# Performance work log

Hardware: AMD Instinct MI355X
Metric: run time of the kernel (lower is better)

## Reference

```python
import jax, jax.numpy as jnp
import numpy as np

B, S, D, H = 4, 2048, 1024, 16
HD = D // H

def setup_inputs() -> dict:
    key = jax.random.key(0)
    ks = jax.random.split(key, 11)
    s = 1.0 / np.sqrt(D)
    def lin(k):
        kw, kb = jax.random.split(k)
        return (jax.random.uniform(kw, (D, D), jnp.float32, -s, s),
                jax.random.uniform(kb, (D,), jnp.float32, -s, s))
    Wq, bq = lin(ks[0]); Wk, bk = lin(ks[1]); Wv, bv = lin(ks[2]); Wo, bo = lin(ks[3])
    return {
        "query": jax.random.normal(ks[4], (B, S, D), jnp.float32),
        "key": jax.random.normal(ks[5], (B, S, D), jnp.float32),
        "value": jax.random.normal(ks[6], (B, S, D), jnp.float32),
        "Wq": Wq, "bq": bq, "Wk": Wk, "bk": bk,
        "Wv": Wv, "bv": bv, "Wo": Wo, "bo": bo,
    }

def reference(query, key, value, Wq, bq, Wk, bk, Wv, bv, Wo, bo):
    def split_heads(x):  # [B,S,D] -> [B,H,S,HD]
        return x.reshape(B, S, H, HD).transpose(0, 2, 1, 3)
    q = split_heads(query @ Wq + bq)
    k = split_heads(key @ Wk + bk)
    v = split_heads(value @ Wv + bv)
    scores = jnp.einsum('bhqd,bhkd->bhqk', q, k) / np.sqrt(HD)
    probs = jax.nn.softmax(scores, axis=-1)
    ctx = jnp.einsum('bhqk,bhkd->bhqd', probs, v)
    ctx = ctx.transpose(0, 2, 1, 3).reshape(B, S, D)
    return ctx @ Wo + bo
```

## Files before the change

### kernel.cpp

```cpp
#include <hip/hip_runtime.h>
#include <hip/hip_bf16.h>

#define B_ 4
#define S_ 2048
#define D_ 1024
#define H_ 16
#define HD_ 64
#define M_ (B_*S_)

typedef __bf16 bf16;
typedef bf16 bf16x8 __attribute__((ext_vector_type(8)));
typedef bf16 bf16x4 __attribute__((ext_vector_type(4)));
typedef bf16 bf16x2 __attribute__((ext_vector_type(2)));
typedef float f32x4 __attribute__((ext_vector_type(4)));
typedef unsigned u32x4 __attribute__((ext_vector_type(4)));

__device__ __forceinline__ void gload_lds16(const void* g, void* l) {
  __builtin_amdgcn_global_load_lds((const __attribute__((address_space(1))) void*)g,
                                   (__attribute__((address_space(3))) void*)l, 16, 0, 0);
}

__device__ __forceinline__ unsigned pk2(float a, float b) {
  bf16x2 v;
  v[0] = (bf16)a; v[1] = (bf16)b;
  return __builtin_bit_cast(unsigned, v);
}

#define CVT_BLKS (M_ * D_ / 2048)

__global__ __launch_bounds__(256)
void prep_kernel(const float* __restrict__ q, const float* __restrict__ k,
                 const float* __restrict__ v,
                 bf16* __restrict__ qo, bf16* __restrict__ ko, bf16* __restrict__ vo,
                 const float* __restrict__ Wq, const float* __restrict__ Wk,
                 const float* __restrict__ Wv, const float* __restrict__ Wo,
                 bf16* __restrict__ Wqt, bf16* __restrict__ Wkt,
                 bf16* __restrict__ Wvt, bf16* __restrict__ Wot) {
  __shared__ float tile[64][65];
  const int bid = blockIdx.x;
  if (bid < 3 * CVT_BLKS) {
    const int slice = bid / CVT_BLKS, bx = bid % CVT_BLKS;
    const float* src; bf16* dst;
    if (slice == 0)      { src = q; dst = qo; }
    else if (slice == 1) { src = k; dst = ko; }
    else                 { src = v; dst = vo; }
    size_t i = ((size_t)bx * 256 + threadIdx.x) * 8;
    f32x4 a = *(const f32x4*)(src + i);
    f32x4 b = *(const f32x4*)(src + i + 4);
    bf16x8 o;
    o[0] = (bf16)a[0]; o[1] = (bf16)a[1]; o[2] = (bf16)a[2]; o[3] = (bf16)a[3];
    o[4] = (bf16)b[0]; o[5] = (bf16)b[1]; o[6] = (bf16)b[2]; o[7] = (bf16)b[3];
    *(bf16x8*)(dst + i) = o;
  } else {
    const int wb = bid - 3 * CVT_BLKS;
    const int z = wb >> 8, t = wb & 255;
    const float* W; bf16* Wt;
    switch (z) {
      case 0: W = Wq; Wt = Wqt; break;
      case 1: W = Wk; Wt = Wkt; break;
      case 2: W = Wv; Wt = Wvt; break;
      default: W = Wo; Wt = Wot; break;
    }
    const int n0 = (t & 15) * 64, k0 = (t >> 4) * 64;
    const int tx = threadIdx.x & 63, ty = threadIdx.x >> 6;
#pragma unroll
    for (int i = 0; i < 16; i++) {
      int kk = ty + i * 4;
      tile[kk][tx] = W[(size_t)(k0 + kk) * D_ + n0 + tx];
    }
    __syncthreads();
#pragma unroll
    for (int i = 0; i < 16; i++) {
      int n = ty + i * 4;
      Wt[(size_t)(n0 + n) * D_ + k0 + tx] = (bf16)tile[tx][n];
    }
  }
}

#define QSCALE 0.18033688011112042f

__global__ __launch_bounds__(256)
void proj_gemm_kernel(const bf16* __restrict__ Aqb, const bf16* __restrict__ Akb,
                      const bf16* __restrict__ Avb,
                      const bf16* __restrict__ Wqt, const bf16* __restrict__ Wkt,
                      const bf16* __restrict__ Wvt,
                      const float* __restrict__ bq, const float* __restrict__ bk,
                      const float* __restrict__ bv,
                      bf16* __restrict__ qb, bf16* __restrict__ kb, bf16* __restrict__ vbT) {
  __shared__ bf16 As[2][128 * 64];
  __shared__ bf16 Bs[2][128 * 64];
  const bf16* A; const bf16* Bt; const float* bias;
  if (blockIdx.z == 0)      { A = Aqb; Bt = Wqt; bias = bq; }
  else if (blockIdx.z == 1) { A = Akb; Bt = Wkt; bias = bk; }
  else                      { A = Avb; Bt = Wvt; bias = bv; }

  const int orig = blockIdx.y * gridDim.x + blockIdx.x;
  const int swz  = (orig & 7) * 64 + (orig >> 3);
  const int n0 = (swz & 7) * 128, m0 = (swz >> 3) * 128;

  const int tid = threadIdx.x;
  const int lane = tid & 63, w = tid >> 6;
  const int wr = w >> 1, wc = w & 1;
  const int l15 = lane & 15, quad = lane >> 4;
  const int srow = lane >> 3, schunk = lane & 7;

  f32x4 acc[4][4] = {};

  auto stage = [&](int buf, int kt) {
    const int k0 = kt * 64;
#pragma unroll
    for (int t = 0; t < 4; t++) {
      int r0 = w * 32 + t * 8;
      int row = r0 + srow;
      int cg = schunk ^ (row & 7);
      gload_lds16(A + (size_t)(m0 + row) * D_ + k0 + cg * 8, &As[buf][r0 * 64]);
      gload_lds16(Bt + (size_t)(n0 + row) * D_ + k0 + cg * 8, &Bs[buf][r0 * 64]);
    }
  };

  auto compute = [&](int cur) {
#pragma unroll
    for (int ks = 0; ks < 2; ks++) {
      bf16x8 a[4], b[4];
#pragma unroll
      for (int fm = 0; fm < 4; fm++) {
        int row = wr * 64 + fm * 16 + l15;
        a[fm] = *(const bf16x8*)(&As[cur][row * 64 + (((ks * 4 + quad) ^ (row & 7)) * 8)]);
      }
#pragma unroll
      for (int fn = 0; fn < 4; fn++) {
        int row = wc * 64 + fn * 16 + l15;
        b[fn] = *(const bf16x8*)(&Bs[cur][row * 64 + (((ks * 4 + quad) ^ (row & 7)) * 8)]);
      }
#pragma unroll
      for (int fm = 0; fm < 4; fm++)
#pragma unroll
        for (int fn = 0; fn < 4; fn++)
          acc[fm][fn] = __builtin_amdgcn_mfma_f32_16x16x32_bf16(a[fm], b[fn], acc[fm][fn], 0, 0, 0);
    }
  };

  constexpr int KT = D_ / 64;
  stage(0, 0);
  __syncthreads();
  for (int kt = 0; kt < KT; kt++) {
    if (kt + 1 < KT) stage((kt + 1) & 1, kt + 1);
    compute(kt & 1);
    __syncthreads();
  }

  if (blockIdx.z < 2) {
    bf16* C = (blockIdx.z == 0) ? qb : kb;
    float scale = (blockIdx.z == 0) ? QSCALE : 1.0f;
#pragma unroll
    for (int fm = 0; fm < 4; fm++) {
      int row = m0 + wr * 64 + fm * 16 + quad * 4;
#pragma unroll
      for (int fn = 0; fn < 4; fn++) {
        int col = n0 + wc * 64 + fn * 16 + l15;
        float bval = bias[col];
#pragma unroll
        for (int r = 0; r < 4; r++)
          C[(size_t)(row + r) * D_ + col] = (bf16)((acc[fm][fn][r] + bval) * scale);
      }
    }
  } else {
#pragma unroll
    for (int fm = 0; fm < 4; fm++) {
      int row = m0 + wr * 64 + fm * 16 + quad * 4;
#pragma unroll
      for (int fn = 0; fn < 4; fn++) {
        int col = n0 + wc * 64 + fn * 16 + l15;
        float bval = bias[col];
        bf16x4 pk;
#pragma unroll
        for (int r = 0; r < 4; r++) pk[r] = (bf16)(acc[fm][fn][r] + bval);
        *(bf16x4*)(vbT + (size_t)col * M_ + row) = pk;
      }
    }
  }
}

#define NT_ (S_ / 64)

__global__ __launch_bounds__(256)
void attn_kernel(const bf16* __restrict__ qb, const bf16* __restrict__ kb,
                 const bf16* __restrict__ vbT, bf16* __restrict__ ctxb) {
  __shared__ bf16 Ks[2][64 * 64];
  __shared__ bf16 Vs[3][64 * 64];

  const int orig = blockIdx.y * gridDim.x + blockIdx.x;
  const int swz  = (orig & 7) * 128 + (orig >> 3);
  const int bh = swz >> 4;
  const int b = bh >> 4, h = bh & 15;
  const int q0 = (swz & 15) * 128;

  const int tid = threadIdx.x, lane = tid & 63, w = tid >> 6;
  const int l15 = lane & 15, quad = lane >> 4;

  const size_t baseQ = ((size_t)(b * S_ + q0)) * D_ + h * HD_;

  bf16x8 qf[2][2];
#pragma unroll
  for (int fm = 0; fm < 2; fm++)
#pragma unroll
    for (int ks = 0; ks < 2; ks++)
      qf[fm][ks] = *(const bf16x8*)(qb + baseQ + (size_t)(w * 32 + fm * 16 + l15) * D_ + ks * 32 + quad * 8);

  bf16x8 vones;
#pragma unroll
  for (int i = 0; i < 8; i++) vones[i] = (bf16)1.0f;

  f32x4 o[2][4] = {};
  f32x4 o_l[2] = {};

  const int srow_i = lane >> 3;
  const int schunk = lane & 7;

  auto stage = [&](int kt) {
    if (kt >= NT_) return;
    const int kbuf = kt & 1, vbuf = kt % 3;
#pragma unroll
    for (int t = 0; t < 2; t++) {
      const int r0 = w * 16 + t * 8;
      const int row = r0 + srow_i;
      const int c = schunk ^ (row & 7);
      const bf16* gK = kb + ((size_t)(b * S_ + kt * 64 + row)) * D_ + h * 64 + c * 8;
      gload_lds16(gK, &Ks[kbuf][r0 * 64]);
      const bf16* gV = vbT + ((size_t)(h * 64 + row)) * M_ + b * S_ + kt * 64 + c * 8;
      gload_lds16(gV, &Vs[vbuf][r0 * 64]);
    }
  };

  auto QK = [&](f32x4 (&st)[4][2], int kbuf) {
#pragma unroll
    for (int fk = 0; fk < 4; fk++)
#pragma unroll
      for (int fq = 0; fq < 2; fq++) st[fk][fq] = f32x4{};
    __builtin_amdgcn_s_setprio(1);
#pragma unroll
    for (int ks = 0; ks < 2; ks++) {
#pragma unroll
      for (int fk = 0; fk < 4; fk++) {
        const int key = fk * 16 + l15;
        bf16x8 kf = *(const bf16x8*)(&Ks[kbuf][key * 64 + (((ks * 4 + quad) ^ (key & 7)) * 8)]);
#pragma unroll
        for (int fq = 0; fq < 2; fq++)
          st[fk][fq] = __builtin_amdgcn_mfma_f32_16x16x32_bf16(kf, qf[fq][ks], st[fk][fq], 0, 0, 0);
      }
    }
    __builtin_amdgcn_s_setprio(0);
  };

  auto FIN = [&](f32x4 (&st)[4][2], int vbuf) {
#pragma unroll
    for (int fk = 0; fk < 4; fk++)
#pragma unroll
      for (int fq = 0; fq < 2; fq++) {
        st[fk][fq][0] = __builtin_amdgcn_exp2f(st[fk][fq][0]);
        st[fk][fq][1] = __builtin_amdgcn_exp2f(st[fk][fq][1]);
        st[fk][fq][2] = __builtin_amdgcn_exp2f(st[fk][fq][2]);
        st[fk][fq][3] = __builtin_amdgcn_exp2f(st[fk][fq][3]);
      }
#pragma unroll
    for (int ks2 = 0; ks2 < 2; ks2++) {
      bf16x8 pf[2], vf[4];
#pragma unroll
      for (int fm = 0; fm < 2; fm++) {
        unsigned A0 = pk2(st[2 * ks2][fm][0], st[2 * ks2][fm][1]);
        unsigned A1 = pk2(st[2 * ks2][fm][2], st[2 * ks2][fm][3]);
        unsigned B0 = pk2(st[2 * ks2 + 1][fm][0], st[2 * ks2 + 1][fm][1]);
        unsigned B1 = pk2(st[2 * ks2 + 1][fm][2], st[2 * ks2 + 1][fm][3]);
        auto s0 = __builtin_amdgcn_permlane32_swap(A0, B0, false, false);
        auto s1 = __builtin_amdgcn_permlane32_swap(A1, B1, false, false);
        auto t0 = __builtin_amdgcn_permlane16_swap(s0[0], s0[1], false, false);
        auto t1 = __builtin_amdgcn_permlane16_swap(s1[0], s1[1], false, false);
        u32x4 wv;
        wv[0] = t0[0]; wv[1] = t1[0]; wv[2] = t0[1]; wv[3] = t1[1];
        pf[fm] = __builtin_bit_cast(bf16x8, wv);
      }
#pragma unroll
      for (int fd = 0; fd < 4; fd++) {
        const int d = fd * 16 + l15;
        vf[fd] = *(const bf16x8*)(&Vs[vbuf][d * 64 + (((ks2 * 4 + quad) ^ (d & 7)) * 8)]);
      }
      __builtin_amdgcn_s_setprio(1);
#pragma unroll
      for (int fm = 0; fm < 2; fm++) {
#pragma unroll
        for (int fd = 0; fd < 4; fd++)
          o[fm][fd] = __builtin_amdgcn_mfma_f32_16x16x32_bf16(pf[fm], vf[fd], o[fm][fd], 0, 0, 0);
        o_l[fm] = __builtin_amdgcn_mfma_f32_16x16x32_bf16(pf[fm], vones, o_l[fm], 0, 0, 0);
      }
      __builtin_amdgcn_s_setprio(0);
    }
  };

  f32x4 stA[4][2], stB[4][2];

  stage(0);
  __syncthreads();

  for (int i = 0; i < NT_ / 2; i++) {
    const int t = 2 * i;
    stage(t + 1);
    QK(stA, t & 1);
    if (i > 0) FIN(stB, (t - 1) % 3);
    __syncthreads();
    stage(t + 2);
    QK(stB, (t + 1) & 1);
    FIN(stA, t % 3);
    __syncthreads();
  }
  FIN(stB, (NT_ - 1) % 3);

#pragma unroll
  for (int fm = 0; fm < 2; fm++) {
#pragma unroll
    for (int r = 0; r < 4; r++) {
      float inv = 1.0f / o_l[fm][r];
      int row = w * 32 + fm * 16 + quad * 4 + r;
#pragma unroll
      for (int fd = 0; fd < 4; fd++)
        ctxb[baseQ + (size_t)row * D_ + fd * 16 + l15] = (bf16)(o[fm][fd][r] * inv);
    }
  }
}

__global__ __launch_bounds__(256)
void out_gemm_kernel(const bf16* __restrict__ A, const bf16* __restrict__ Bt,
                     const float* __restrict__ bias, float* __restrict__ Cout) {
  __shared__ bf16 As[2][128 * 64];
  __shared__ bf16 Bs[2][128 * 64];
  const int orig = blockIdx.y * gridDim.x + blockIdx.x;
  const int swz  = (orig & 7) * 64 + (orig >> 3);
  const int n0 = (swz & 7) * 128, m0 = (swz >> 3) * 128;

  const int tid = threadIdx.x;
  const int lane = tid & 63, w = tid >> 6;
  const int wr = w >> 1, wc = w & 1;
  const int l15 = lane & 15, quad = lane >> 4;
  const int srow = lane >> 3, schunk = lane & 7;

  f32x4 acc[4][4] = {};

  auto stage = [&](int buf, int kt) {
    const int k0 = kt * 64;
#pragma unroll
    for (int t = 0; t < 4; t++) {
      int r0 = w * 32 + t * 8;
      int row = r0 + srow;
      int cg = schunk ^ (row & 7);
      gload_lds16(A + (size_t)(m0 + row) * D_ + k0 + cg * 8, &As[buf][r0 * 64]);
      gload_lds16(Bt + (size_t)(n0 + row) * D_ + k0 + cg * 8, &Bs[buf][r0 * 64]);
    }
  };

  auto compute = [&](int cur) {
#pragma unroll
    for (int ks = 0; ks < 2; ks++) {
      bf16x8 a[4], b[4];
#pragma unroll
      for (int fm = 0; fm < 4; fm++) {
        int row = wr * 64 + fm * 16 + l15;
        a[fm] = *(const bf16x8*)(&As[cur][row * 64 + (((ks * 4 + quad) ^ (row & 7)) * 8)]);
      }
#pragma unroll
      for (int fn = 0; fn < 4; fn++) {
        int row = wc * 64 + fn * 16 + l15;
        b[fn] = *(const bf16x8*)(&Bs[cur][row * 64 + (((ks * 4 + quad) ^ (row & 7)) * 8)]);
      }
#pragma unroll
      for (int fm = 0; fm < 4; fm++)
#pragma unroll
        for (int fn = 0; fn < 4; fn++)
          acc[fm][fn] = __builtin_amdgcn_mfma_f32_16x16x32_bf16(a[fm], b[fn], acc[fm][fn], 0, 0, 0);
    }
  };

  constexpr int KT = D_ / 64;
  stage(0, 0);
  __syncthreads();
  for (int kt = 0; kt < KT; kt++) {
    if (kt + 1 < KT) stage((kt + 1) & 1, kt + 1);
    compute(kt & 1);
    __syncthreads();
  }

#pragma unroll
  for (int fm = 0; fm < 4; fm++) {
    int row = m0 + wr * 64 + fm * 16 + quad * 4;
#pragma unroll
    for (int fn = 0; fn < 4; fn++) {
      int col = n0 + wc * 64 + fn * 16 + l15;
      float bval = bias[col];
#pragma unroll
      for (int r = 0; r < 4; r++)
        Cout[(size_t)(row + r) * D_ + col] = acc[fm][fn][r] + bval;
    }
  }
}

extern "C" void kernel_launch(void* const* d_in, const int* in_sizes, int n_in,
                              void* d_out, int out_size, void* d_ws, size_t ws_size,
                              hipStream_t stream) {
  const float* query = (const float*)d_in[0];
  const float* key   = (const float*)d_in[1];
  const float* value = (const float*)d_in[2];
  const float* Wq = (const float*)d_in[3];
  const float* bq = (const float*)d_in[4];
  const float* Wk = (const float*)d_in[5];
  const float* bk = (const float*)d_in[6];
  const float* Wv = (const float*)d_in[7];
  const float* bv = (const float*)d_in[8];
  const float* Wo = (const float*)d_in[9];
  const float* bo = (const float*)d_in[10];
  float* out = (float*)d_out;

  char* ws = (char*)d_ws;
  const size_t WT_BYTES = (size_t)D_ * D_ * sizeof(bf16);
  const size_t MD_BYTES = (size_t)M_ * D_ * sizeof(bf16);
  bf16* Wqt  = (bf16*)(ws);
  bf16* Wkt  = (bf16*)(ws + WT_BYTES);
  bf16* Wvt  = (bf16*)(ws + 2 * WT_BYTES);
  bf16* Wot  = (bf16*)(ws + 3 * WT_BYTES);
  bf16* qb   = (bf16*)(ws + 4 * WT_BYTES);
  bf16* kb   = (bf16*)(ws + 4 * WT_BYTES + MD_BYTES);
  bf16* vbT  = (bf16*)(ws + 4 * WT_BYTES + 2 * MD_BYTES);
  bf16* ctxb = (bf16*)(ws + 4 * WT_BYTES + 3 * MD_BYTES);
  bf16* qcv  = ctxb;
  bf16* kcv  = (bf16*)(ws + 4 * WT_BYTES + 4 * MD_BYTES);
  bf16* vcv  = (bf16*)(ws + 4 * WT_BYTES + 5 * MD_BYTES);

  prep_kernel<<<3 * CVT_BLKS + 1024, 256, 0, stream>>>(
      query, key, value, qcv, kcv, vcv,
      Wq, Wk, Wv, Wo, Wqt, Wkt, Wvt, Wot);

  proj_gemm_kernel<<<dim3(D_ / 128, M_ / 128, 3), 256, 0, stream>>>(
      qcv, kcv, vcv, Wqt, Wkt, Wvt, bq, bk, bv, qb, kb, vbT);

  attn_kernel<<<dim3(S_ / 128, B_ * H_), 256, 0, stream>>>(qb, kb, vbT, ctxb);

  out_gemm_kernel<<<dim3(D_ / 128, M_ / 128), 256, 0, stream>>>(ctxb, Wot, bo, out);
}
```

Before: 336.2 us.

## Rework QKV projection GEMM into 256x256 tiles with 8-wave phased pipeline

The projection GEMM moves from 128x128 tiles with 4 waves to 256x256 tiles with 8 waves. The K loop now interleaves LDS fragment loads, quarter-tile global-to-LDS staging and MFMA bursts behind fine-grained barriers, explicit vmcnt waits and s_setprio around the MFMA blocks. The goal is more data reuse per LDS byte and better overlap of memory traffic with matrix math. In exchange it uses much larger LDS, more accumulator registers and a grid of only 384 blocks, which can hurt occupancy and tail balance.

```diff
diff --git a/kernel.cpp b/kernel.cpp
--- a/kernel.cpp
+++ b/kernel.cpp
@@ -79,7 +79,7 @@
 
 #define QSCALE 0.18033688011112042f
 
-__global__ __launch_bounds__(256)
+__global__ __launch_bounds__(512, 2)
 void proj_gemm_kernel(const bf16* __restrict__ Aqb, const bf16* __restrict__ Akb,
                       const bf16* __restrict__ Avb,
                       const bf16* __restrict__ Wqt, const bf16* __restrict__ Wkt,
@@ -87,94 +87,156 @@
                       const float* __restrict__ bq, const float* __restrict__ bk,
                       const float* __restrict__ bv,
                       bf16* __restrict__ qb, bf16* __restrict__ kb, bf16* __restrict__ vbT) {
-  __shared__ bf16 As[2][128 * 64];
-  __shared__ bf16 Bs[2][128 * 64];
+  __shared__ bf16 As[2][256 * 64];
+  __shared__ bf16 Bs[2][256 * 64];
   const bf16* A; const bf16* Bt; const float* bias;
   if (blockIdx.z == 0)      { A = Aqb; Bt = Wqt; bias = bq; }
   else if (blockIdx.z == 1) { A = Akb; Bt = Wkt; bias = bk; }
   else                      { A = Avb; Bt = Wvt; bias = bv; }
 
   const int orig = blockIdx.y * gridDim.x + blockIdx.x;
-  const int swz  = (orig & 7) * 64 + (orig >> 3);
-  const int n0 = (swz & 7) * 128, m0 = (swz >> 3) * 128;
+  const int swz  = (orig & 7) * 16 + (orig >> 3);
+  const int n0 = (swz & 3) * 256, m0 = (swz >> 2) * 256;
 
   const int tid = threadIdx.x;
   const int lane = tid & 63, w = tid >> 6;
-  const int wr = w >> 1, wc = w & 1;
+  const int wm = w >> 2, wn = w & 3;
   const int l15 = lane & 15, quad = lane >> 4;
-  const int srow = lane >> 3, schunk = lane & 7;
-
-  f32x4 acc[4][4] = {};
-
-  auto stage = [&](int buf, int kt) {
-    const int k0 = kt * 64;
-#pragma unroll
-    for (int t = 0; t < 4; t++) {
-      int r0 = w * 32 + t * 8;
-      int row = r0 + srow;
-      int cg = schunk ^ (row & 7);
-      gload_lds16(A + (size_t)(m0 + row) * D_ + k0 + cg * 8, &As[buf][r0 * 64]);
-      gload_lds16(Bt + (size_t)(n0 + row) * D_ + k0 + cg * 8, &Bs[buf][r0 * 64]);
-    }
-  };
-
-  auto compute = [&](int cur) {
-#pragma unroll
-    for (int ks = 0; ks < 2; ks++) {
-      bf16x8 a[4], b[4];
-#pragma unroll
-      for (int fm = 0; fm < 4; fm++) {
-        int row = wr * 64 + fm * 16 + l15;
-        a[fm] = *(const bf16x8*)(&As[cur][row * 64 + (((ks * 4 + quad) ^ (row & 7)) * 8)]);
-      }
-#pragma unroll
-      for (int fn = 0; fn < 4; fn++) {
-        int row = wc * 64 + fn * 16 + l15;
-        b[fn] = *(const bf16x8*)(&Bs[cur][row * 64 + (((ks * 4 + quad) ^ (row & 7)) * 8)]);
-      }
-#pragma unroll
-      for (int fm = 0; fm < 4; fm++)
-#pragma unroll
-        for (int fn = 0; fn < 4; fn++)
-          acc[fm][fn] = __builtin_amdgcn_mfma_f32_16x16x32_bf16(a[fm], b[fn], acc[fm][fn], 0, 0, 0);
-    }
-  };
+
+  f32x4 acc[8][4] = {};
+  bf16x8 a[4][2];
+  bf16x8 b[2][2][2];
+
+  auto stA = [&](int buf, int kt, int rb) {
+    int row = rb + w * 8 + (lane >> 3);
+    int cg = (lane & 7) ^ (row & 7);
+    gload_lds16(A + (size_t)(m0 + row) * D_ + kt * 64 + cg * 8,
+                &As[buf][(rb + w * 8) * 64]);
+  };
+  auto stB = [&](int buf, int kt, int rb) {
+    int row = rb + w * 8 + (lane >> 3);
+    int cg = (lane & 7) ^ (row & 7);
+    gload_lds16(Bt + (size_t)(n0 + row) * D_ + kt * 64 + cg * 8,
+                &Bs[buf][(rb + w * 8) * 64]);
+  };
+  auto uAe = [&](int buf, int kt) { stA(buf, kt, 0);  stA(buf, kt, 128); };
+  auto uAl = [&](int buf, int kt) { stA(buf, kt, 64); stA(buf, kt, 192); };
+  auto uBa = [&](int buf, int kt) { stB(buf, kt, 0);  stB(buf, kt, 128); };
+  auto uBb = [&](int buf, int kt) { stB(buf, kt, 64); stB(buf, kt, 192); };
+
+  auto loadA = [&](int c, int qm) {
+#pragma unroll
+    for (int fm = 0; fm < 4; fm++)
+#pragma unroll
+      for (int ks = 0; ks < 2; ks++) {
+        int row = wm * 128 + qm * 64 + fm * 16 + l15;
+        a[fm][ks] = *(const bf16x8*)(&As[c][row * 64 + (((ks * 4 + quad) ^ (row & 7)) * 8)]);
+      }
+  };
+  auto loadB = [&](int c, int qn) {
+#pragma unroll
+    for (int fn = 0; fn < 2; fn++)
+#pragma unroll
+      for (int ks = 0; ks < 2; ks++) {
+        int row = wn * 64 + qn * 32 + fn * 16 + l15;
+        b[qn][fn][ks] = *(const bf16x8*)(&Bs[c][row * 64 + (((ks * 4 + quad) ^ (row & 7)) * 8)]);
+      }
+  };
+  auto mma = [&](int qm, int qn) {
+    __builtin_amdgcn_s_setprio(1);
+#pragma unroll
+    for (int fm = 0; fm < 4; fm++)
+#pragma unroll
+      for (int fn = 0; fn < 2; fn++)
+#pragma unroll
+        for (int ks = 0; ks < 2; ks++)
+          acc[qm * 4 + fm][qn * 2 + fn] = __builtin_amdgcn_mfma_f32_16x16x32_bf16(
+              a[fm][ks], b[qn][fn][ks], acc[qm * 4 + fm][qn * 2 + fn], 0, 0, 0);
+    __builtin_amdgcn_s_setprio(0);
+  };
+
+#define PH_SYNC() do { \
+    __builtin_amdgcn_s_barrier(); \
+    asm volatile("s_waitcnt lgkmcnt(0)" ::: "memory"); \
+    __builtin_amdgcn_sched_barrier(0); \
+  } while (0)
 
   constexpr int KT = D_ / 64;
-  stage(0, 0);
-  __syncthreads();
-  for (int kt = 0; kt < KT; kt++) {
-    if (kt + 1 < KT) stage((kt + 1) & 1, kt + 1);
-    compute(kt & 1);
-    __syncthreads();
-  }
+  constexpr int NI = KT / 2;
+
+  uAe(0, 0); uBa(0, 0); uAl(0, 0); uBb(0, 0);
+  uAe(1, 1); uBa(1, 1); uAl(1, 1);
+  asm volatile("s_waitcnt vmcnt(6)" ::: "memory");
+  __builtin_amdgcn_s_barrier();
+
+  for (int i = 0; i < NI; i++) {
+    const int t1 = 2 * i + 1, t2 = 2 * i + 2, t3 = 2 * i + 3;
+    loadA(0, 0); loadB(0, 0);
+    uBb(1, t1);
+    PH_SYNC(); mma(0, 0);
+    __builtin_amdgcn_s_barrier();
+    loadB(0, 1);
+    if (t2 < KT) uAe(0, t2);
+    PH_SYNC(); mma(0, 1);
+    __builtin_amdgcn_s_barrier();
+    loadA(0, 1);
+    if (t2 < KT) uBa(0, t2);
+    PH_SYNC(); mma(1, 0);
+    __builtin_amdgcn_s_barrier();
+    if (t2 < KT) uAl(0, t2);
+    __builtin_amdgcn_s_barrier();
+    __builtin_amdgcn_sched_barrier(0);
+    mma(1, 1);
+    if (i + 1 < NI) { asm volatile("s_waitcnt vmcnt(6)" ::: "memory"); }
+    else            { asm volatile("s_waitcnt vmcnt(0)" ::: "memory"); }
+    __builtin_amdgcn_s_barrier();
+    loadA(1, 0); loadB(1, 0);
+    if (t2 < KT) uBb(0, t2);
+    PH_SYNC(); mma(0, 0);
+    __builtin_amdgcn_s_barrier();
+    loadB(1, 1);
+    if (t3 < KT) uAe(1, t3);
+    PH_SYNC(); mma(0, 1);
+    __builtin_amdgcn_s_barrier();
+    loadA(1, 1);
+    if (t3 < KT) uBa(1, t3);
+    PH_SYNC(); mma(1, 0);
+    __builtin_amdgcn_s_barrier();
+    if (t3 < KT) uAl(1, t3);
+    __builtin_amdgcn_s_barrier();
+    __builtin_amdgcn_sched_barrier(0);
+    mma(1, 1);
+    if (i + 1 < NI) { asm volatile("s_waitcnt vmcnt(6)" ::: "memory"); }
+    __builtin_amdgcn_s_barrier();
+  }
+#undef PH_SYNC
 
   if (blockIdx.z < 2) {
     bf16* C = (blockIdx.z == 0) ? qb : kb;
     float scale = (blockIdx.z == 0) ? QSCALE : 1.0f;
 #pragma unroll
-    for (int fm = 0; fm < 4; fm++) {
-      int row = m0 + wr * 64 + fm * 16 + quad * 4;
-#pragma unroll
-      for (int fn = 0; fn < 4; fn++) {
-        int col = n0 + wc * 64 + fn * 16 + l15;
+    for (int fmk = 0; fmk < 8; fmk++) {
+      int row = m0 + wm * 128 + fmk * 16 + quad * 4;
+#pragma unroll
+      for (int fnk = 0; fnk < 4; fnk++) {
+        int col = n0 + wn * 64 + fnk * 16 + l15;
         float bval = bias[col];
 #pragma unroll
         for (int r = 0; r < 4; r++)
-          C[(size_t)(row + r) * D_ + col] = (bf16)((acc[fm][fn][r] + bval) * scale);
+          C[(size_t)(row + r) * D_ + col] = (bf16)((acc[fmk][fnk][r] + bval) * scale);
       }
     }
   } else {
 #pragma unroll
-    for (int fm = 0; fm < 4; fm++) {
-      int row = m0 + wr * 64 + fm * 16 + quad * 4;
-#pragma unroll
-      for (int fn = 0; fn < 4; fn++) {
-        int col = n0 + wc * 64 + fn * 16 + l15;
+    for (int fmk = 0; fmk < 8; fmk++) {
+      int row = m0 + wm * 128 + fmk * 16 + quad * 4;
+#pragma unroll
+      for (int fnk = 0; fnk < 4; fnk++) {
+        int col = n0 + wn * 64 + fnk * 16 + l15;
         float bval = bias[col];
         bf16x4 pk;
 #pragma unroll
-        for (int r = 0; r < 4; r++) pk[r] = (bf16)(acc[fm][fn][r] + bval);
+        for (int r = 0; r < 4; r++) pk[r] = (bf16)(acc[fmk][fnk][r] + bval);
         *(bf16x4*)(vbT + (size_t)col * M_ + row) = pk;
       }
     }
@@ -436,7 +498,7 @@
       query, key, value, qcv, kcv, vcv,
       Wq, Wk, Wv, Wo, Wqt, Wkt, Wvt, Wot);
 
-  proj_gemm_kernel<<<dim3(D_ / 128, M_ / 128, 3), 256, 0, stream>>>(
+  proj_gemm_kernel<<<dim3(D_ / 256, M_ / 256, 3), 512, 0, stream>>>(
       qcv, kcv, vcv, Wqt, Wkt, Wvt, bq, bk, bv, qb, kb, vbT);
 
   attn_kernel<<<dim3(S_ / 128, B_ * H_), 256, 0, stream>>>(qb, kb, vbT, ctxb);
```

Result: slower. 345.9 us (+2.9%).
